# Performance work log

Hardware: AMD Instinct MI355X
Metric: run time of the kernel (lower is better)

The kernel has to match this reference:

```python
import jax, jax.numpy as jnp
import numpy as np

B, L, E, H = 8, 2048, 256, 4
D = E // H  # head_dim = 64


def setup_inputs() -> dict:
    key = jax.random.key(0)
    k1, k2, k3, k4, k5 = jax.random.split(key, 5)
    x = jax.random.normal(k1, (B, L, E), dtype=jnp.float32)
    # torch.nn.MultiheadAttention packed in-projection: weight [3E, E], bias [3E]
    lim = float(np.sqrt(6.0 / (3 * E + E)))  # xavier_uniform on [3E, E]
    in_proj_w = jax.random.uniform(k2, (3 * E, E), dtype=jnp.float32, minval=-lim, maxval=lim)
    in_proj_b = jnp.zeros((3 * E,), dtype=jnp.float32)
    # W_gnn: xavier_uniform on [E, E]; B_gnn: randn [E]
    limw = float(np.sqrt(6.0 / (E + E)))
    W_gnn = jax.random.uniform(k3, (E, E), dtype=jnp.float32, minval=-limw, maxval=limw)
    B_gnn = jax.random.normal(k4, (E,), dtype=jnp.float32)
    return {"x": x, "in_proj_w": in_proj_w, "in_proj_b": in_proj_b,
            "W_gnn": W_gnn, "B_gnn": B_gnn}


def reference(x, in_proj_w, in_proj_b, W_gnn, B_gnn):
    # --- MultiheadAttention(x, x, x), batch_first=True, need_weights=True ---
    qkv = x @ in_proj_w.T + in_proj_b                      # [B, L, 3E]
    q, k, v = jnp.split(qkv, 3, axis=-1)                   # each [B, L, E]
    # split heads -> [B, H, L, D]
    q = q.reshape(B, L, H, D).transpose(0, 2, 1, 3)
    k = k.reshape(B, L, H, D).transpose(0, 2, 1, 3)
    scale = 1.0 / jnp.sqrt(jnp.float32(D))
    scores = jnp.einsum('bhqd,bhkd->bhqk', q * scale, k)   # [B, H, L, L]
    attn = jax.nn.softmax(scores, axis=-1)
    # need_weights=True (average_attn_weights default True): head-averaged probs
    b = attn.mean(axis=1)                                  # [B, L, L]
    # NOTE: MHA output `a` (out_proj(attn @ v)) is discarded by the module,
    # so out_proj / value path do not affect the result.
    # --- x = bmm(b, x) @ W_gnn + B_gnn ---
    agg = jnp.einsum('bql,bld->bqd', b, x)                 # [B, L, E]
    return agg @ W_gnn + B_gnn
```

## Files before the change

### kernel.cpp

```cpp
#include <hip/hip_runtime.h>

#define B_ 8
#define L_ 2048
#define E_ 256
#define H_ 4
#define D_ 64

typedef __bf16 bf16;
typedef __bf16 bf16x8 __attribute__((ext_vector_type(8)));
typedef __bf16 bf16x4 __attribute__((ext_vector_type(4)));
typedef float  f32x4  __attribute__((ext_vector_type(4)));
typedef float  f32x16 __attribute__((ext_vector_type(16)));

#define QSCALE 0.1803368801111244f

__device__ __forceinline__ float fexp2(float x) { return __builtin_amdgcn_exp2f(x); }
__device__ __forceinline__ float flog2(float x) { return __builtin_amdgcn_logf(x); }

__device__ __forceinline__ void barrier_lds() {
    asm volatile("s_waitcnt lgkmcnt(0)" ::: "memory");
    __builtin_amdgcn_s_barrier();
}

__global__ void prep_kernel(const float* __restrict__ x,
                            const float* __restrict__ in_proj_w,
                            const float* __restrict__ W_gnn,
                            bf16* __restrict__ xb, bf16* __restrict__ Wcat) {
    int bid = blockIdx.x;
    if (bid < 4096) {
        size_t i = ((size_t)bid * 256 + threadIdx.x) * 4;
        f32x4 v = *(const f32x4*)&x[i];
        bf16x4 o;
#pragma unroll
        for (int j = 0; j < 4; j++) o[j] = (bf16)v[j];
        *(bf16x4*)&xb[i] = o;
    } else {
        int r = bid - 4096;
        int e = threadIdx.x;
        float v = (r < 512) ? in_proj_w[r * E_ + e] : W_gnn[e * E_ + (r - 512)];
        Wcat[r * E_ + e] = (bf16)v;
    }
}

__global__ __launch_bounds__(256, 2) void proj_kernel(
    const bf16* __restrict__ xb, const bf16* __restrict__ Wcat,
    const float* __restrict__ in_proj_b, const float* __restrict__ B_gnn,
    bf16* __restrict__ Qs, bf16* __restrict__ Ks, bf16* __restrict__ XWT) {
    __shared__ bf16 ldsW[2][256 * 36];
    int tid  = threadIdx.x;
    int lane = tid & 63, wave = tid >> 6;
    int l16  = lane & 15, quad = lane >> 4;
    int m0 = blockIdx.x * 64 + wave * 16;
    int by = blockIdx.y;
    int n0 = by * 256;

    f32x4 acc[16];
#pragma unroll
    for (int i = 0; i < 16; i++) acc[i] = (f32x4){0.f, 0.f, 0.f, 0.f};

    bf16x8 af[8];
    const bf16* xrow = xb + (size_t)(m0 + l16) * E_;
#pragma unroll
    for (int ks = 0; ks < 8; ks++) af[ks] = *(const bf16x8*)&xrow[ks * 32 + quad * 8];

    const bf16* Wb = Wcat + (size_t)n0 * E_;

#pragma unroll
    for (int it = 0; it < 4; it++) {
        int idx = it * 256 + tid;
        int n = idx >> 2, c8 = (idx & 3) * 8;
        *(bf16x8*)&ldsW[0][n * 36 + c8] = *(const bf16x8*)&Wb[(size_t)n * E_ + c8];
    }
    __syncthreads();

    int cur = 0;
    for (int ks = 0; ks < 8; ks++) {
        bf16x8 pw[4];
        if (ks < 7) {
#pragma unroll
            for (int it = 0; it < 4; it++) {
                int idx = it * 256 + tid;
                int n = idx >> 2, c8 = (idx & 3) * 8;
                pw[it] = *(const bf16x8*)&Wb[(size_t)n * E_ + (ks + 1) * 32 + c8];
            }
        }
#pragma unroll
        for (int nt = 0; nt < 16; nt++) {
            bf16x8 bfv = *(const bf16x8*)&ldsW[cur][(nt * 16 + l16) * 36 + quad * 8];
            acc[nt] = __builtin_amdgcn_mfma_f32_16x16x32_bf16(af[ks], bfv, acc[nt], 0, 0, 0);
        }
        if (ks < 7) {
#pragma unroll
            for (int it = 0; it < 4; it++) {
                int idx = it * 256 + tid;
                int n = idx >> 2, c8 = (idx & 3) * 8;
                *(bf16x8*)&ldsW[cur ^ 1][n * 36 + c8] = pw[it];
            }
        }
        barrier_lds();
        cur ^= 1;
    }

#pragma unroll
    for (int nt = 0; nt < 16; nt++) {
        int n = n0 + nt * 16 + l16;
        if (by == 0) {
            float bias = in_proj_b[n];
#pragma unroll
            for (int r = 0; r < 4; r++) {
                int m = m0 + quad * 4 + r;
                Qs[(size_t)m * E_ + n] = (bf16)((acc[nt][r] + bias) * QSCALE);
            }
        } else if (by == 1) {
            float bias = in_proj_b[n];
            int col = n - 256;
#pragma unroll
            for (int r = 0; r < 4; r++) {
                int m = m0 + quad * 4 + r;
                Ks[(size_t)m * E_ + col] = (bf16)(acc[nt][r] + bias);
            }
        } else {
            int nc = n - 512;
            float bias = B_gnn[nc];
            int m = m0 + quad * 4;
            int b = m >> 11, l = m & 2047;
            bf16x4 pk;
#pragma unroll
            for (int r = 0; r < 4; r++) pk[r] = (bf16)(acc[nt][r] + bias);
            *(bf16x4*)&XWT[((size_t)b * E_ + nc) * L_ + l] = pk;
        }
    }
}

__global__ __launch_bounds__(256, 4) void stats_kernel(
    const bf16* __restrict__ Qs, const bf16* __restrict__ Ks,
    float* __restrict__ o) {
    __shared__ bf16 ldsK[2][128 * 72];
    int tid  = threadIdx.x;
    int lane = tid & 63, wave = tid >> 6;
    int r32  = lane & 31, half = lane >> 5;
    int qt = blockIdx.x, h = blockIdx.y, b = blockIdx.z;
    int q0 = qt * 128 + wave * 32;

    bf16x8 qa[4];
    const bf16* qrow = Qs + ((size_t)b * L_ + q0 + r32) * E_ + h * D_;
#pragma unroll
    for (int c = 0; c < 4; c++) qa[c] = *(const bf16x8*)&qrow[c * 16 + half * 8];

    float lsum[16];
#pragma unroll
    for (int i = 0; i < 16; i++) lsum[i] = 0.f;

    const bf16* Kb = Ks + (size_t)b * L_ * E_ + h * D_;

#pragma unroll
    for (int it = 0; it < 4; it++) {
        int idx = it * 256 + tid;
        int key = idx >> 3, dc = (idx & 7) * 8;
        *(bf16x8*)&ldsK[0][key * 72 + dc] =
            *(const bf16x8*)&Kb[(size_t)key * E_ + dc];
    }
    __syncthreads();

    int cur = 0;
    for (int kt = 0; kt < 16; kt++) {
        bf16x8 pk[4];
        if (kt < 15) {
#pragma unroll
            for (int it = 0; it < 4; it++) {
                int idx = it * 256 + tid;
                pk[it] = *(const bf16x8*)&Kb[(size_t)((kt + 1) * 128 + (idx >> 3)) * E_ + (idx & 7) * 8];
            }
        }
#pragma unroll
        for (int nt = 0; nt < 4; nt++) {
            f32x16 S = {};
#pragma unroll
            for (int c = 0; c < 4; c++) {
                bf16x8 kb = *(const bf16x8*)&ldsK[cur][(nt * 32 + r32) * 72 + c * 16 + half * 8];
                S = __builtin_amdgcn_mfma_f32_32x32x16_bf16(qa[c], kb, S, 0, 0, 0);
            }
#pragma unroll
            for (int i = 0; i < 16; i++) lsum[i] += fexp2(S[i]);
        }
        if (kt < 15) {
#pragma unroll
            for (int it = 0; it < 4; it++) {
                int idx = it * 256 + tid;
                *(bf16x8*)&ldsK[cur ^ 1][(idx >> 3) * 72 + (idx & 7) * 8] = pk[it];
            }
        }
        barrier_lds();
        cur ^= 1;
    }
#pragma unroll
    for (int i = 0; i < 16; i++) {
        float v = lsum[i];
        v += __shfl_xor(v, 1); v += __shfl_xor(v, 2); v += __shfl_xor(v, 4);
        v += __shfl_xor(v, 8); v += __shfl_xor(v, 16);
        lsum[i] = v;
    }
    if (r32 == 0) {
        float* op = o + ((size_t)(b * H_ + h)) * L_ + q0;
#pragma unroll
        for (int i = 0; i < 16; i++) {
            int row = (i & 3) + 8 * (i >> 2) + 4 * half;
            op[row] = -(2.0f + flog2(lsum[i]));
        }
    }
}

__global__ __launch_bounds__(256, 2) void pass2_kernel(
    const bf16* __restrict__ Qs, const bf16* __restrict__ Ks,
    const bf16* __restrict__ XWT, const float* __restrict__ o,
    float* __restrict__ Opart) {
    __shared__ alignas(16) unsigned char smem[79872];
    bf16* ldsK  = (bf16*)smem;
    bf16* ldsXW = (bf16*)(smem + 33792);
    bf16* ldsP  = (bf16*)(smem + 70656);

    int tid  = threadIdx.x;
    int lane = tid & 63, wave = tid >> 6;
    int l32  = lane & 31, half = lane >> 5;
    int qh = wave & 1, kh = wave >> 1;
    int nh = kh;

    int flat = blockIdx.x;
    int b   = flat & 7;
    int qt  = (flat >> 3) & 31;
    int ksp = flat >> 8;

    int qw = qt * 64 + qh * 32 + l32;

    bf16x8 qf[4][4];
    const bf16* qrow = Qs + ((size_t)b * L_ + qw) * E_;
#pragma unroll
    for (int h = 0; h < H_; h++)
#pragma unroll
        for (int c = 0; c < 4; c++)
            qf[h][c] = *(const bf16x8*)&qrow[h * 64 + c * 16 + half * 8];

    float oh[4];
#pragma unroll
    for (int h = 0; h < H_; h++)
        oh[h] = o[((size_t)(b * H_ + h)) * L_ + qw];

    f32x16 zero = {};
    f32x16 acc[4];
#pragma unroll
    for (int i = 0; i < 4; i++) acc[i] = zero;

    const bf16* Kb = Ks + (size_t)b * L_ * E_;
    const bf16* Xb = XWT + (size_t)b * E_ * L_;

    {
        int k0 = ksp * 1024;
#pragma unroll
        for (int it = 0; it < 8; it++) {
            int idx = it * 256 + tid;
            int key = idx >> 5, col = (idx & 31) * 8;
            *(bf16x8*)&ldsK[key * 264 + col] =
                *(const bf16x8*)&Kb[(size_t)(k0 + key) * E_ + col];
        }
#pragma unroll
        for (int it = 0; it < 8; it++) {
            int idx = it * 256 + tid;
            int n = idx >> 3, kc = (idx & 7) * 8;
            *(bf16x8*)&ldsXW[n * 72 + kc] =
                *(const bf16x8*)&Xb[(size_t)n * L_ + k0 + kc];
        }
    }
    __syncthreads();

    for (int kt = 0; kt < 16; kt++) {
        bf16x8 pkf[8], pxf[8];
        if (kt < 15) {
            int k1 = ksp * 1024 + (kt + 1) * 64;
#pragma unroll
            for (int it = 0; it < 8; it++) {
                int idx = it * 256 + tid;
                int key = idx >> 5, col = (idx & 31) * 8;
                pkf[it] = *(const bf16x8*)&Kb[(size_t)(k1 + key) * E_ + col];
            }
#pragma unroll
            for (int it = 0; it < 8; it++) {
                int idx = it * 256 + tid;
                int n = idx >> 3, kc = (idx & 7) * 8;
                pxf[it] = *(const bf16x8*)&Xb[(size_t)n * L_ + k1 + kc];
            }
        }

        f32x16 P = zero;
#pragma unroll
        for (int h = 0; h < H_; h++) {
            f32x16 s = zero;
#pragma unroll
            for (int c = 0; c < 4; c++) {
                bf16x8 ka = *(const bf16x8*)&ldsK[(kh * 32 + l32) * 264 + h * 64 + c * 16 + half * 8];
                s = __builtin_amdgcn_mfma_f32_32x32x16_bf16(ka, qf[h][c], s, 0, 0, 0);
            }
#pragma unroll
            for (int r = 0; r < 16; r++) P[r] += fexp2(s[r] + oh[h]);
        }

#pragma unroll
        for (int g = 0; g < 4; g++) {
            bf16x4 pk;
#pragma unroll
            for (int j = 0; j < 4; j++) pk[j] = (bf16)P[4 * g + j];
            *(bf16x4*)&ldsP[(qh * 32 + l32) * 72 + kh * 32 + g * 8 + half * 4] = pk;
        }
        barrier_lds();

#pragma unroll
        for (int kc = 0; kc < 4; kc++) {
            bf16x8 pa = *(const bf16x8*)&ldsP[(qh * 32 + l32) * 72 + kc * 16 + half * 8];
#pragma unroll
            for (int nt = 0; nt < 4; nt++) {
                bf16x8 xw = *(const bf16x8*)&ldsXW[(nh * 128 + nt * 32 + l32) * 72 + kc * 16 + half * 8];
                acc[nt] = __builtin_amdgcn_mfma_f32_32x32x16_bf16(pa, xw, acc[nt], 0, 0, 0);
            }
        }
        barrier_lds();

        if (kt < 15) {
#pragma unroll
            for (int it = 0; it < 8; it++) {
                int idx = it * 256 + tid;
                int key = idx >> 5, col = (idx & 31) * 8;
                *(bf16x8*)&ldsK[key * 264 + col] = pkf[it];
            }
#pragma unroll
            for (int it = 0; it < 8; it++) {
                int idx = it * 256 + tid;
                int n = idx >> 3, kc = (idx & 7) * 8;
                *(bf16x8*)&ldsXW[n * 72 + kc] = pxf[it];
            }
            barrier_lds();
        }
    }

    float* Ob = Opart + ((size_t)ksp * B_ + b) * (size_t)L_ * E_
              + (size_t)(qt * 64 + qh * 32) * E_ + nh * 128;
#pragma unroll
    for (int nt = 0; nt < 4; nt++)
#pragma unroll
        for (int r = 0; r < 16; r++) {
            int row = (r & 3) + 8 * (r >> 2) + 4 * half;
            Ob[(size_t)row * E_ + nt * 32 + l32] = acc[nt][r];
        }
}

__global__ void reduce_kernel(const float* __restrict__ Op, float* __restrict__ out) {
    size_t i = ((size_t)blockIdx.x * 256 + threadIdx.x) * 4;
    const size_t BLE = (size_t)B_ * L_ * E_;
    f32x4 a = *(const f32x4*)&Op[i];
    f32x4 c = *(const f32x4*)&Op[BLE + i];
#pragma unroll
    for (int j = 0; j < 4; j++) a[j] += c[j];
    *(f32x4*)&out[i] = a;
}

extern "C" void kernel_launch(void* const* d_in, const int* in_sizes, int n_in,
                              void* d_out, int out_size, void* d_ws, size_t ws_size,
                              hipStream_t stream) {
    const float* x   = (const float*)d_in[0];
    const float* ipw = (const float*)d_in[1];
    const float* ipb = (const float*)d_in[2];
    const float* wg  = (const float*)d_in[3];
    const float* bg  = (const float*)d_in[4];

    char* ws = (char*)d_ws;
    bf16*  Qs    = (bf16*)(ws);
    bf16*  Ks    = (bf16*)(ws + 8388608);
    bf16*  XWT   = (bf16*)(ws + 16777216);
    float* o     = (float*)(ws + 25165824);
    float* Opart = (float*)(ws + 25427968);
    bf16*  xb    = (bf16*)(ws + 25427968);
    bf16*  Wcat  = (bf16*)(ws + 33816576);

    prep_kernel<<<4864, 256, 0, stream>>>(x, ipw, wg, xb, Wcat);
    proj_kernel<<<dim3(256, 3), 256, 0, stream>>>(xb, Wcat, ipb, bg, Qs, Ks, XWT);
    stats_kernel<<<dim3(16, 4, 8), 256, 0, stream>>>(Qs, Ks, o);
    pass2_kernel<<<512, 256, 0, stream>>>(Qs, Ks, XWT, o, Opart);
    reduce_kernel<<<4096, 256, 0, stream>>>(Opart, (float*)d_out);
}
```

Baseline: 184.8 us.

## Warp-specialize pass2 into producer/consumer waves and drop split-K reduce

The pass2 kernel moves to 512-thread blocks. Four waves compute scores, exp and the P tile, and also load XW. The other four waves run the P·XW MFMA accumulation one tile behind and prefetch K. Double-buffered LDS (about 156KB) connects the two groups. The key-dimension split and the separate reduce kernel are removed, so each block covers all 2048 keys and writes the output directly. This saves the partial-output round trip and one launch, but halves the grid to 256 blocks and allows only one block per CU because of the LDS size.

```diff
diff --git a/kernel.cpp b/kernel.cpp
--- a/kernel.cpp
+++ b/kernel.cpp
@@ -210,155 +210,167 @@
     }
 }
 
-__global__ __launch_bounds__(256, 2) void pass2_kernel(
+__global__ void __launch_bounds__(512) __attribute__((amdgpu_waves_per_eu(2, 2)))
+pass2_kernel(
     const bf16* __restrict__ Qs, const bf16* __restrict__ Ks,
     const bf16* __restrict__ XWT, const float* __restrict__ o,
-    float* __restrict__ Opart) {
-    __shared__ alignas(16) unsigned char smem[79872];
-    bf16* ldsK  = (bf16*)smem;
-    bf16* ldsXW = (bf16*)(smem + 33792);
-    bf16* ldsP  = (bf16*)(smem + 70656);
+    float* __restrict__ out) {
+    __shared__ alignas(16) unsigned char smem[159744];
+    bf16* ldsK0  = (bf16*)smem;
+    bf16* ldsK1  = (bf16*)(smem + 33792);
+    bf16* ldsXW0 = (bf16*)(smem + 67584);
+    bf16* ldsXW1 = (bf16*)(smem + 104448);
+    bf16* ldsP0  = (bf16*)(smem + 141312);
+    bf16* ldsP1  = (bf16*)(smem + 150528);
 
     int tid  = threadIdx.x;
     int lane = tid & 63, wave = tid >> 6;
     int l32  = lane & 31, half = lane >> 5;
-    int qh = wave & 1, kh = wave >> 1;
-    int nh = kh;
 
     int flat = blockIdx.x;
-    int b   = flat & 7;
-    int qt  = (flat >> 3) & 31;
-    int ksp = flat >> 8;
-
-    int qw = qt * 64 + qh * 32 + l32;
-
-    bf16x8 qf[4][4];
-    const bf16* qrow = Qs + ((size_t)b * L_ + qw) * E_;
-#pragma unroll
-    for (int h = 0; h < H_; h++)
-#pragma unroll
-        for (int c = 0; c < 4; c++)
-            qf[h][c] = *(const bf16x8*)&qrow[h * 64 + c * 16 + half * 8];
-
-    float oh[4];
-#pragma unroll
-    for (int h = 0; h < H_; h++)
-        oh[h] = o[((size_t)(b * H_ + h)) * L_ + qw];
-
-    f32x16 zero = {};
-    f32x16 acc[4];
-#pragma unroll
-    for (int i = 0; i < 4; i++) acc[i] = zero;
+    int b  = flat & 7;
+    int qt = flat >> 3;
+    int q0 = qt * 64;
 
     const bf16* Kb = Ks + (size_t)b * L_ * E_;
     const bf16* Xb = XWT + (size_t)b * E_ * L_;
 
-    {
-        int k0 = ksp * 1024;
-#pragma unroll
-        for (int it = 0; it < 8; it++) {
-            int idx = it * 256 + tid;
-            int key = idx >> 5, col = (idx & 31) * 8;
-            *(bf16x8*)&ldsK[key * 264 + col] =
-                *(const bf16x8*)&Kb[(size_t)(k0 + key) * E_ + col];
-        }
-#pragma unroll
-        for (int it = 0; it < 8; it++) {
-            int idx = it * 256 + tid;
-            int n = idx >> 3, kc = (idx & 7) * 8;
-            *(bf16x8*)&ldsXW[n * 72 + kc] =
-                *(const bf16x8*)&Xb[(size_t)n * L_ + k0 + kc];
-        }
+#pragma unroll
+    for (int it = 0; it < 4; it++) {
+        int idx = it * 512 + tid;
+        int key = idx >> 5, col = (idx & 31) * 8;
+        *(bf16x8*)&ldsK0[key * 264 + col] =
+            *(const bf16x8*)&Kb[(size_t)key * E_ + col];
     }
     __syncthreads();
 
-    for (int kt = 0; kt < 16; kt++) {
-        bf16x8 pkf[8], pxf[8];
-        if (kt < 15) {
-            int k1 = ksp * 1024 + (kt + 1) * 64;
+    if (wave < 4) {
+        int pqh = wave & 1, pkh = wave >> 1;
+        int qw = q0 + pqh * 32 + l32;
+
+        bf16x8 qf[4][4];
+        const bf16* qrow = Qs + ((size_t)b * L_ + qw) * E_;
+#pragma unroll
+        for (int h = 0; h < H_; h++)
+#pragma unroll
+            for (int c = 0; c < 4; c++)
+                qf[h][c] = *(const bf16x8*)&qrow[h * 64 + c * 16 + half * 8];
+
+        float oh[4];
+#pragma unroll
+        for (int h = 0; h < H_; h++)
+            oh[h] = o[((size_t)(b * H_ + h)) * L_ + qw];
+
+        f32x16 zero = {};
+        for (int kt = 0; kt < 32; kt++) {
+            bf16* kcur = (kt & 1) ? ldsK1  : ldsK0;
+            bf16* xcur = (kt & 1) ? ldsXW1 : ldsXW0;
+            bf16* pcur = (kt & 1) ? ldsP1  : ldsP0;
+
+            bf16x8 pxf[8];
 #pragma unroll
             for (int it = 0; it < 8; it++) {
                 int idx = it * 256 + tid;
-                int key = idx >> 5, col = (idx & 31) * 8;
-                pkf[it] = *(const bf16x8*)&Kb[(size_t)(k1 + key) * E_ + col];
-            }
+                int n = idx >> 3, kc8 = (idx & 7) * 8;
+                pxf[it] = *(const bf16x8*)&Xb[(size_t)n * L_ + kt * 64 + kc8];
+            }
+
+            f32x16 P = zero;
+#pragma unroll
+            for (int h = 0; h < H_; h++) {
+                f32x16 s = zero;
+#pragma unroll
+                for (int c = 0; c < 4; c++) {
+                    bf16x8 ka = *(const bf16x8*)&kcur[(pkh * 32 + l32) * 264 + h * 64 + c * 16 + half * 8];
+                    s = __builtin_amdgcn_mfma_f32_32x32x16_bf16(ka, qf[h][c], s, 0, 0, 0);
+                }
+#pragma unroll
+                for (int r = 0; r < 16; r++) P[r] += fexp2(s[r] + oh[h]);
+            }
+
+#pragma unroll
+            for (int g = 0; g < 4; g++) {
+                bf16x4 pk;
+#pragma unroll
+                for (int j = 0; j < 4; j++) pk[j] = (bf16)P[4 * g + j];
+                *(bf16x4*)&pcur[(pqh * 32 + l32) * 72 + pkh * 32 + g * 8 + half * 4] = pk;
+            }
+
 #pragma unroll
             for (int it = 0; it < 8; it++) {
                 int idx = it * 256 + tid;
-                int n = idx >> 3, kc = (idx & 7) * 8;
-                pxf[it] = *(const bf16x8*)&Xb[(size_t)n * L_ + k1 + kc];
-            }
-        }
-
-        f32x16 P = zero;
-#pragma unroll
-        for (int h = 0; h < H_; h++) {
-            f32x16 s = zero;
-#pragma unroll
-            for (int c = 0; c < 4; c++) {
-                bf16x8 ka = *(const bf16x8*)&ldsK[(kh * 32 + l32) * 264 + h * 64 + c * 16 + half * 8];
-                s = __builtin_amdgcn_mfma_f32_32x32x16_bf16(ka, qf[h][c], s, 0, 0, 0);
-            }
-#pragma unroll
-            for (int r = 0; r < 16; r++) P[r] += fexp2(s[r] + oh[h]);
-        }
-
-#pragma unroll
-        for (int g = 0; g < 4; g++) {
-            bf16x4 pk;
-#pragma unroll
-            for (int j = 0; j < 4; j++) pk[j] = (bf16)P[4 * g + j];
-            *(bf16x4*)&ldsP[(qh * 32 + l32) * 72 + kh * 32 + g * 8 + half * 4] = pk;
-        }
-        barrier_lds();
+                int n = idx >> 3, kc8 = (idx & 7) * 8;
+                *(bf16x8*)&xcur[n * 72 + kc8] = pxf[it];
+            }
+            barrier_lds();
+        }
+    } else {
+        int cw = wave - 4;
+        int cqh = cw & 1, cnh = cw >> 1;
+        int ctid = tid - 256;
+
+        f32x16 zero = {};
+        f32x16 acc[4];
+#pragma unroll
+        for (int i = 0; i < 4; i++) acc[i] = zero;
+
+        for (int kt = 0; kt < 32; kt++) {
+            bf16* knext = (kt & 1) ? ldsK0  : ldsK1;
+            bf16* xprev = (kt & 1) ? ldsXW0 : ldsXW1;
+            bf16* pprev = (kt & 1) ? ldsP0  : ldsP1;
+
+            bf16x8 pkf[8];
+            if (kt < 31) {
+#pragma unroll
+                for (int it = 0; it < 8; it++) {
+                    int idx = it * 256 + ctid;
+                    int key = idx >> 5, col = (idx & 31) * 8;
+                    pkf[it] = *(const bf16x8*)&Kb[(size_t)((kt + 1) * 64 + key) * E_ + col];
+                }
+            }
+
+            if (kt > 0) {
+#pragma unroll
+                for (int kc = 0; kc < 4; kc++) {
+                    bf16x8 pa = *(const bf16x8*)&pprev[(cqh * 32 + l32) * 72 + kc * 16 + half * 8];
+#pragma unroll
+                    for (int nt = 0; nt < 4; nt++) {
+                        bf16x8 xw = *(const bf16x8*)&xprev[(cnh * 128 + nt * 32 + l32) * 72 + kc * 16 + half * 8];
+                        acc[nt] = __builtin_amdgcn_mfma_f32_32x32x16_bf16(pa, xw, acc[nt], 0, 0, 0);
+                    }
+                }
+            }
+
+            if (kt < 31) {
+#pragma unroll
+                for (int it = 0; it < 8; it++) {
+                    int idx = it * 256 + ctid;
+                    int key = idx >> 5, col = (idx & 31) * 8;
+                    *(bf16x8*)&knext[key * 264 + col] = pkf[it];
+                }
+            }
+            barrier_lds();
+        }
 
 #pragma unroll
         for (int kc = 0; kc < 4; kc++) {
-            bf16x8 pa = *(const bf16x8*)&ldsP[(qh * 32 + l32) * 72 + kc * 16 + half * 8];
+            bf16x8 pa = *(const bf16x8*)&ldsP1[(cqh * 32 + l32) * 72 + kc * 16 + half * 8];
 #pragma unroll
             for (int nt = 0; nt < 4; nt++) {
-                bf16x8 xw = *(const bf16x8*)&ldsXW[(nh * 128 + nt * 32 + l32) * 72 + kc * 16 + half * 8];
+                bf16x8 xw = *(const bf16x8*)&ldsXW1[(cnh * 128 + nt * 32 + l32) * 72 + kc * 16 + half * 8];
                 acc[nt] = __builtin_amdgcn_mfma_f32_32x32x16_bf16(pa, xw, acc[nt], 0, 0, 0);
             }
         }
-        barrier_lds();
-
-        if (kt < 15) {
-#pragma unroll
-            for (int it = 0; it < 8; it++) {
-                int idx = it * 256 + tid;
-                int key = idx >> 5, col = (idx & 31) * 8;
-                *(bf16x8*)&ldsK[key * 264 + col] = pkf[it];
-            }
-#pragma unroll
-            for (int it = 0; it < 8; it++) {
-                int idx = it * 256 + tid;
-                int n = idx >> 3, kc = (idx & 7) * 8;
-                *(bf16x8*)&ldsXW[n * 72 + kc] = pxf[it];
-            }
-            barrier_lds();
-        }
-    }
-
-    float* Ob = Opart + ((size_t)ksp * B_ + b) * (size_t)L_ * E_
-              + (size_t)(qt * 64 + qh * 32) * E_ + nh * 128;
-#pragma unroll
-    for (int nt = 0; nt < 4; nt++)
-#pragma unroll
-        for (int r = 0; r < 16; r++) {
-            int row = (r & 3) + 8 * (r >> 2) + 4 * half;
-            Ob[(size_t)row * E_ + nt * 32 + l32] = acc[nt][r];
-        }
-}
-
-__global__ void reduce_kernel(const float* __restrict__ Op, float* __restrict__ out) {
-    size_t i = ((size_t)blockIdx.x * 256 + threadIdx.x) * 4;
-    const size_t BLE = (size_t)B_ * L_ * E_;
-    f32x4 a = *(const f32x4*)&Op[i];
-    f32x4 c = *(const f32x4*)&Op[BLE + i];
-#pragma unroll
-    for (int j = 0; j < 4; j++) a[j] += c[j];
-    *(f32x4*)&out[i] = a;
+
+        float* Ob = out + ((size_t)b * L_ + q0 + cqh * 32) * E_ + cnh * 128;
+#pragma unroll
+        for (int nt = 0; nt < 4; nt++)
+#pragma unroll
+            for (int r = 0; r < 16; r++) {
+                int row = (r & 3) + 8 * (r >> 2) + 4 * half;
+                Ob[(size_t)row * E_ + nt * 32 + l32] = acc[nt][r];
+            }
+    }
 }
 
 extern "C" void kernel_launch(void* const* d_in, const int* in_sizes, int n_in,
@@ -371,17 +383,15 @@
     const float* bg  = (const float*)d_in[4];
 
     char* ws = (char*)d_ws;
-    bf16*  Qs    = (bf16*)(ws);
-    bf16*  Ks    = (bf16*)(ws + 8388608);
-    bf16*  XWT   = (bf16*)(ws + 16777216);
-    float* o     = (float*)(ws + 25165824);
-    float* Opart = (float*)(ws + 25427968);
-    bf16*  xb    = (bf16*)(ws + 25427968);
-    bf16*  Wcat  = (bf16*)(ws + 33816576);
+    bf16*  Qs   = (bf16*)(ws);
+    bf16*  Ks   = (bf16*)(ws + 8388608);
+    bf16*  XWT  = (bf16*)(ws + 16777216);
+    float* o    = (float*)(ws + 25165824);
+    bf16*  xb   = (bf16*)(ws + 25427968);
+    bf16*  Wcat = (bf16*)(ws + 33816576);
 
     prep_kernel<<<4864, 256, 0, stream>>>(x, ipw, wg, xb, Wcat);
     proj_kernel<<<dim3(256, 3), 256, 0, stream>>>(xb, Wcat, ipb, bg, Qs, Ks, XWT);
     stats_kernel<<<dim3(16, 4, 8), 256, 0, stream>>>(Qs, Ks, o);
-    pass2_kernel<<<512, 256, 0, stream>>>(Qs, Ks, XWT, o, Opart);
-    reduce_kernel<<<4096, 256, 0, stream>>>(Opart, (float*)d_out);
-}
+    pass2_kernel<<<256, 512, 0, stream>>>(Qs, Ks, XWT, o, (float*)d_out);
+}
```

Measured after the change: 174.7 us. 1.06x faster.
